# Kernel tuning notes

Measured on AMD Instinct MI355X. Metric: run time of the kernel, lower is better.

Reference implementation:

```python
import jax, jax.numpy as jnp
import numpy as np
import math

B, S, D = 2, 2048, 1024
H, HKV, HD = 16, 4, 64
SF = 4
SD = HD // SF  # sparsity proj dim = 16
TEMP = 1.0
INIT_STD = 0.02


def rope(qk):
    # qk: [b, h, s, d]
    d = qk.shape[-1]
    theta = 1.0 / (10000.0 ** (jnp.arange(0, d, 2, dtype=jnp.float32) / d))  # [d/2]
    s = jnp.arange(qk.shape[2], dtype=jnp.float32)
    freqs = jnp.outer(s, theta)                     # [s, d/2]
    freqs = jnp.concatenate([freqs, freqs], -1)     # [s, d]
    qk1, qk2 = jnp.split(qk, 2, axis=-1)
    rot = jnp.concatenate([-qk2, qk1], -1)
    return qk * jnp.cos(freqs) + rot * jnp.sin(freqs)


def setup_inputs() -> dict:
    key = jax.random.key(0)
    ks = jax.random.split(key, 8)
    x = jax.random.normal(ks[0], (B, S, D), dtype=jnp.float32)
    Wq = jax.random.normal(ks[1], (D, D), dtype=jnp.float32) * INIT_STD
    Wk = jax.random.normal(ks[2], (HKV * HD, D), dtype=jnp.float32) * INIT_STD
    Wv = jax.random.normal(ks[3], (HKV * HD, D), dtype=jnp.float32) * INIT_STD
    Wo = jax.random.normal(ks[4], (D, D), dtype=jnp.float32) * INIT_STD
    bo = jnp.zeros((D,), dtype=jnp.float32)
    Ws = jax.random.normal(ks[5], (SD, HD), dtype=jnp.float32) * INIT_STD
    bs = jnp.zeros((SD,), dtype=jnp.float32)
    return {"x": x, "Wq": Wq, "Wk": Wk, "Wv": Wv, "Wo": Wo, "bo": bo, "Ws": Ws, "bs": bs}


def reference(x, Wq, Wk, Wv, Wo, bo, Ws, bs):
    b, s, _ = x.shape
    # projections (torch Linear: x @ W.T)
    q = (x @ Wq.T).reshape(b, s, H, HD).transpose(0, 2, 1, 3)     # [b,H,s,hd]
    k = (x @ Wk.T).reshape(b, s, HKV, HD).transpose(0, 2, 1, 3)   # [b,Hkv,s,hd]
    v = (x @ Wv.T).reshape(b, s, HKV, HD).transpose(0, 2, 1, 3)
    q = rope(q)
    k = rope(k)
    n_rep = H // HKV
    k = jnp.repeat(k, n_rep, axis=1)  # [b,H,s,hd]
    v = jnp.repeat(v, n_rep, axis=1)
    # low-rank sparsity gate
    q_sp = q @ Ws.T + bs              # [b,H,s,sd]
    k_sp = k @ Ws.T + bs
    sp_scores = jnp.einsum('bhid,bhjd->bhij', q_sp, k_sp) / math.sqrt(SD)
    gate = jax.nn.sigmoid(sp_scores / TEMP)
    attn = jnp.einsum('bhid,bhjd->bhij', q, k) / math.sqrt(HD)
    attn = attn * gate
    causal = jnp.triu(jnp.ones((s, s), dtype=bool), k=1)
    attn = jnp.where(causal, -jnp.inf, attn)
    w = jax.nn.softmax(attn, axis=-1)
    out = jnp.einsum('bhij,bhjd->bhid', w, v)               # [b,H,s,hd]
    out = out.transpose(0, 2, 1, 3).reshape(b, s, H * HD)   # [b,s,D]
    return out @ Wo.T + bo
```

## Files before the change

kernel.cpp:

```cpp
#include <hip/hip_runtime.h>
#include <math.h>

#define B_ 2
#define S_ 2048
#define D_ 1024
#define H_ 16
#define HKV_ 4
#define HD_ 64
#define SD_ 16

typedef __attribute__((ext_vector_type(8))) short bf16x8;
typedef __attribute__((ext_vector_type(4))) float f32x4;
typedef __attribute__((ext_vector_type(8))) unsigned short us8;
typedef __attribute__((ext_vector_type(4))) unsigned short us4;

#define LOG2E 1.4426950408889634f

__device__ __forceinline__ unsigned short f2bf(float f) {
  unsigned int u = __builtin_bit_cast(unsigned int, f);
  u += 0x7fffu + ((u >> 16) & 1u);
  return (unsigned short)(u >> 16);
}

__device__ __forceinline__ void gload16(const unsigned short* g, unsigned short* l) {
  __builtin_amdgcn_global_load_lds(
      (const __attribute__((address_space(1))) unsigned int*)g,
      (__attribute__((address_space(3))) unsigned int*)l, 16, 0, 0);
}

__global__ __launch_bounds__(256) void convert_bf16(
    const float* __restrict__ x, const float* __restrict__ wq,
    const float* __restrict__ wk, const float* __restrict__ wv,
    const float* __restrict__ wo, unsigned short* __restrict__ xb,
    unsigned short* __restrict__ wqkv, unsigned short* __restrict__ wob,
    int* __restrict__ ctr) {
  const int blk = blockIdx.x;
  if (blk == 0 && threadIdx.x == 0) *ctr = 0;
  const float* src;
  unsigned short* dst;
  int off;
  if (blk < 2048)      { src = x;  dst = xb;             off = blk * 2048; }
  else if (blk < 2560) { src = wq; dst = wqkv;           off = (blk - 2048) * 2048; }
  else if (blk < 2688) { src = wk; dst = wqkv + 1048576; off = (blk - 2560) * 2048; }
  else if (blk < 2816) { src = wv; dst = wqkv + 1310720; off = (blk - 2688) * 2048; }
  else                 { src = wo; dst = wob;            off = (blk - 2816) * 2048; }
  const int i = off + threadIdx.x * 8;
  float4 a = *(const float4*)(src + i);
  float4 b = *(const float4*)(src + i + 4);
  us8 o;
  o[0] = f2bf(a.x); o[1] = f2bf(a.y); o[2] = f2bf(a.z); o[3] = f2bf(a.w);
  o[4] = f2bf(b.x); o[5] = f2bf(b.y); o[6] = f2bf(b.z); o[7] = f2bf(b.w);
  *(us8*)(dst + i) = o;
}

__global__ __launch_bounds__(256) void gemm_bf16(
    const unsigned short* __restrict__ A, const unsigned short* __restrict__ Bm,
    const float* __restrict__ bias, float* __restrict__ C, int N) {
  __shared__ unsigned short As[64 * 64];
  __shared__ unsigned short Bs[128 * 64];
  const int tid = threadIdx.x;
  const int w = tid >> 6, lane = tid & 63;
  const int nm = lane & 15, quad = lane >> 4;
  const int m0 = blockIdx.y * 64, n0 = blockIdx.x * 128;
  const int wn = w * 32;

  f32x4 acc[4][2] = {};
  int arow[2], acol[2], brow[4], bcol[4];
#pragma unroll
  for (int it = 0; it < 2; ++it) {
    int s = it * 256 + tid;
    arow[it] = s >> 3;
    acol[it] = ((s & 7) ^ (arow[it] & 7)) * 8;
  }
#pragma unroll
  for (int it = 0; it < 4; ++it) {
    int s = it * 256 + tid;
    brow[it] = s >> 3;
    bcol[it] = ((s & 7) ^ (brow[it] & 7)) * 8;
  }

  for (int k0 = 0; k0 < 1024; k0 += 64) {
    __syncthreads();
#pragma unroll
    for (int it = 0; it < 2; ++it)
      gload16(A + (size_t)(m0 + arow[it]) * 1024 + k0 + acol[it],
              &As[(it * 256 + w * 64) * 8]);
#pragma unroll
    for (int it = 0; it < 4; ++it)
      gload16(Bm + (size_t)(n0 + brow[it]) * 1024 + k0 + bcol[it],
              &Bs[(it * 256 + w * 64) * 8]);
    __syncthreads();

#pragma unroll
    for (int ks = 0; ks < 2; ++ks) {
      const int cq = ks * 4 + quad;
      bf16x8 af[4], bfr[2];
#pragma unroll
      for (int mi = 0; mi < 4; ++mi) {
        const int m = mi * 16 + nm;
        af[mi] = *(const bf16x8*)&As[(m * 8 + (cq ^ (m & 7))) * 8];
      }
#pragma unroll
      for (int ni = 0; ni < 2; ++ni) {
        const int n = wn + ni * 16 + nm;
        bfr[ni] = *(const bf16x8*)&Bs[(n * 8 + (cq ^ (n & 7))) * 8];
      }
#pragma unroll
      for (int mi = 0; mi < 4; ++mi)
#pragma unroll
        for (int ni = 0; ni < 2; ++ni)
          acc[mi][ni] = __builtin_amdgcn_mfma_f32_16x16x32_bf16(
              af[mi], bfr[ni], acc[mi][ni], 0, 0, 0);
    }
  }

  float bv[2] = {0.f, 0.f};
  if (bias) {
#pragma unroll
    for (int ni = 0; ni < 2; ++ni) bv[ni] = bias[n0 + wn + ni * 16 + nm];
  }
#pragma unroll
  for (int mi = 0; mi < 4; ++mi) {
#pragma unroll
    for (int r = 0; r < 4; ++r) {
      const int row = m0 + mi * 16 + quad * 4 + r;
      float* crow = C + (size_t)row * N + n0 + wn + nm;
#pragma unroll
      for (int ni = 0; ni < 2; ++ni) crow[ni * 16] = acc[mi][ni][r] + bv[ni];
    }
  }
}

__global__ __launch_bounds__(256) void rope_scatter(
    const float* __restrict__ P, const float* __restrict__ Ws,
    const float* __restrict__ bs, unsigned short* __restrict__ qh,
    unsigned short* __restrict__ kh, unsigned short* __restrict__ qsp,
    unsigned short* __restrict__ ksp) {
  __shared__ float wsl[16 * 64];
  __shared__ float bsl[16];
  __shared__ float rbuf[4][64];
  const int tid = threadIdx.x;
  const int row = blockIdx.x;
  const int b = row >> 11;
  const int s = row & 2047;
  {
    *(float4*)&wsl[tid * 4] = *(const float4*)&Ws[tid * 4];
    if (tid < 16) bsl[tid] = bs[tid];
  }
  __syncthreads();
  const int w = tid >> 6, lane = tid & 63;
  const int i = lane & 31, halfu = lane >> 5;
  const float theta = powf(10000.f, -((float)(2 * i) * (1.f / 64.f)));
  const float f = (float)s * theta;
  const float cf = cosf(f);
  const float sf = sinf(f);
  for (int slot = w; slot < 20; slot += 4) {
    float val = P[(size_t)row * 1536 + slot * 64 + lane];
    float partner = __shfl_xor(val, 32);
    float rot = halfu ? partner : -partner;
    float r = val * cf + rot * sf;
    unsigned short* dst;
    unsigned short* spdst;
    float qscale, spscale;
    if (slot < 16) {
      dst = qh + ((size_t)(b * 16 + slot) * 2048 + s) * 64;
      spdst = qsp + ((size_t)(b * 16 + slot) * 2048 + s) * 16;
      qscale = 0.125f * LOG2E; spscale = 0.25f * LOG2E;
    } else {
      int hh = slot - 16;
      dst = kh + ((size_t)(b * 4 + hh) * 2048 + s) * 64;
      spdst = ksp + ((size_t)(b * 4 + hh) * 2048 + s) * 16;
      qscale = 1.f; spscale = 1.f;
    }
    dst[lane] = f2bf(r * qscale);
    rbuf[w][lane] = r;
    int p = lane >> 4, j = lane & 15;
    float partial = 0.f;
#pragma unroll
    for (int t = 0; t < 16; ++t)
      partial += wsl[j * 64 + p * 16 + t] * rbuf[w][p * 16 + t];
    partial += __shfl_xor(partial, 16);
    partial += __shfl_xor(partial, 32);
    if (p == 0) spdst[j] = f2bf((partial + bsl[j]) * spscale);
  }
}

__global__ __launch_bounds__(256) void v_transpose(
    const float* __restrict__ proj, unsigned short* __restrict__ vt) {
  __shared__ unsigned short t_[64 * 72];
  const int bkv = blockIdx.y;
  const int s0 = blockIdx.x * 64;
  const int b = bkv >> 2, hkv = bkv & 3;
  const int tid = threadIdx.x;
  const int sl = tid >> 2;
  const int c0 = (tid & 3) * 16;
  const float* src = proj + ((size_t)b * 2048 + s0 + sl) * 1536 + 1280 + hkv * 64 + c0;
  us8 o0, o1;
#pragma unroll
  for (int t = 0; t < 8; ++t) { o0[t] = f2bf(src[t]); o1[t] = f2bf(src[8 + t]); }
  *(us8*)&t_[sl * 72 + c0] = o0;
  *(us8*)&t_[sl * 72 + c0 + 8] = o1;
  __syncthreads();
  const int d = tid >> 2;
  const int sc_ = (tid & 3) * 16;
  us8 w0, w1;
#pragma unroll
  for (int t = 0; t < 8; ++t) w0[t] = t_[(sc_ + t) * 72 + d];
#pragma unroll
  for (int t = 0; t < 8; ++t) w1[t] = t_[(sc_ + 8 + t) * 72 + d];
  unsigned short* dst = vt + (size_t)bkv * 131072 + (size_t)d * 2048 + s0 + sc_;
  *(us8*)dst = w0;
  *(us8*)(dst + 8) = w1;
}

__global__ __launch_bounds__(256) void attn_kernel(
    const unsigned short* __restrict__ qh, const unsigned short* __restrict__ kh,
    const unsigned short* __restrict__ vt, const unsigned short* __restrict__ qsp,
    const unsigned short* __restrict__ ksp, int* __restrict__ ctr,
    unsigned short* __restrict__ ao) {
  __shared__ unsigned short Ks[64 * 64];
  __shared__ unsigned short Vs[64 * 64];
  __shared__ unsigned short Ksp[64 * 16];
  __shared__ unsigned short Pw[4][16 * 64];
  __shared__ int item_s;

  const int tid = threadIdx.x;
  const int w = tid >> 6;
  const int lane = tid & 63;
  const int nm = lane & 15;
  const int quad = lane >> 4;

  int srow_[2], scol_[2];
#pragma unroll
  for (int rd = 0; rd < 2; ++rd) {
    int Lc = rd * 256 + w * 64 + lane;
    int r = Lc >> 3;
    srow_[rd] = r;
    scol_[rd] = ((Lc & 7) ^ (r & 7)) * 8;
  }
  unsigned short* pw = &Pw[w][0];

  for (;;) {
    if (tid == 0) item_s = atomicAdd(ctr, 1);
    __syncthreads();
    const int t = item_s;
    if (t >= 1024) break;
    const int qx = 31 - (t >> 5);
    const int bh = t & 31;
    const int b = bh >> 4, h = bh & 15;
    const int hkv = h >> 2;
    const size_t kbase = (size_t)(b * 4 + hkv) * 2048 * 64;
    const size_t vbase = (size_t)(b * 4 + hkv) * 131072;
    const size_t kspb = (size_t)(b * 4 + hkv) * 2048 * 16;
    const int q0 = qx * 64;
    const int qrow0 = q0 + w * 16;

    const size_t qb = ((size_t)(b * 16 + h) * 2048 + qrow0 + nm) * 64;
    bf16x8 qa0 = *(const bf16x8*)(qh + qb + quad * 8);
    bf16x8 qa1 = *(const bf16x8*)(qh + qb + 32 + quad * 8);
    bf16x8 qspa = {0, 0, 0, 0, 0, 0, 0, 0};
    if (quad < 2)
      qspa = *(const bf16x8*)(qsp + ((size_t)(b * 16 + h) * 2048 + qrow0 + nm) * 16 + quad * 8);

    float l_r[4] = {0.f, 0.f, 0.f, 0.f};
    f32x4 O[4] = {{0.f, 0.f, 0.f, 0.f}, {0.f, 0.f, 0.f, 0.f},
                  {0.f, 0.f, 0.f, 0.f}, {0.f, 0.f, 0.f, 0.f}};

    const int ntile = qx + 1;
    for (int jt = 0; jt < ntile; ++jt) {
      const int j0 = jt * 64;
      __syncthreads();
#pragma unroll
      for (int rd = 0; rd < 2; ++rd) {
        gload16(kh + kbase + (size_t)(j0 + srow_[rd]) * 64 + scol_[rd],
                &Ks[(rd * 256 + w * 64) * 8]);
        gload16(vt + vbase + (size_t)srow_[rd] * 2048 + j0 + scol_[rd],
                &Vs[(rd * 256 + w * 64) * 8]);
      }
      if (w < 2) {
        const int Lc = w * 64 + lane;
        gload16(ksp + kspb + (size_t)(j0 + (Lc >> 1)) * 16 + (Lc & 1) * 8,
                &Ksp[w * 512]);
      }
      __syncthreads();

      const bool needmask = (j0 + 63 > qrow0);
#pragma unroll
      for (int st = 0; st < 4; ++st) {
        const int krow = st * 16 + nm;
        const int r7 = krow & 7;
        bf16x8 kb0 = *(const bf16x8*)&Ks[(krow * 8 + (quad ^ r7)) * 8];
        bf16x8 kb1 = *(const bf16x8*)&Ks[(krow * 8 + ((4 + quad) ^ r7)) * 8];
        bf16x8 gb = *(const bf16x8*)&Ksp[(krow * 2 + (quad & 1)) * 8];
        f32x4 z = {0.f, 0.f, 0.f, 0.f};
        f32x4 s = __builtin_amdgcn_mfma_f32_16x16x32_bf16(qa0, kb0, z, 0, 0, 0);
        s = __builtin_amdgcn_mfma_f32_16x16x32_bf16(qa1, kb1, s, 0, 0, 0);
        f32x4 g = __builtin_amdgcn_mfma_f32_16x16x32_bf16(qspa, gb, z, 0, 0, 0);
#pragma unroll
        for (int r = 0; r < 4; ++r) {
          float gate = 1.f / (1.f + exp2f(-g[r]));
          float v = s[r] * gate;
          if (needmask) {
            const int col = j0 + st * 16 + nm;
            const int rowg = qrow0 + quad * 4 + r;
            v = (col > rowg) ? -INFINITY : v;
          }
          float p = exp2f(v);
          l_r[r] += p;
          const int prow = quad * 4 + r;
          const int chunk = (st * 2 + (nm >> 3)) ^ (prow & 7);
          pw[(prow * 8 + chunk) * 8 + (nm & 7)] = f2bf(p);
        }
      }

#pragma unroll
      for (int c = 0; c < 2; ++c) {
        const int gc = c * 4 + quad;
        bf16x8 pa = *(const bf16x8*)&pw[(nm * 8 + (gc ^ (nm & 7))) * 8];
#pragma unroll
        for (int dt = 0; dt < 4; ++dt) {
          const int vrow = dt * 16 + nm;
          bf16x8 vb = *(const bf16x8*)&Vs[(vrow * 8 + (gc ^ (vrow & 7))) * 8];
          O[dt] = __builtin_amdgcn_mfma_f32_16x16x32_bf16(pa, vb, O[dt], 0, 0, 0);
        }
      }
    }

#pragma unroll
    for (int r = 0; r < 4; ++r) {
      float v = l_r[r];
      v += __shfl_xor(v, 1);
      v += __shfl_xor(v, 2);
      v += __shfl_xor(v, 4);
      v += __shfl_xor(v, 8);
      const float inv = 1.f / v;
      const int rowg = qrow0 + quad * 4 + r;
      unsigned short* orow = ao + ((size_t)b * 2048 + rowg) * 1024 + h * 64 + nm;
#pragma unroll
      for (int dt = 0; dt < 4; ++dt) orow[dt * 16] = f2bf(O[dt][r] * inv);
    }
  }
}

extern "C" void kernel_launch(void* const* d_in, const int* in_sizes, int n_in,
                              void* d_out, int out_size, void* d_ws,
                              size_t ws_size, hipStream_t stream) {
  const float* x = (const float*)d_in[0];
  const float* Wq = (const float*)d_in[1];
  const float* Wk = (const float*)d_in[2];
  const float* Wv = (const float*)d_in[3];
  const float* Wo = (const float*)d_in[4];
  const float* bo = (const float*)d_in[5];
  const float* Ws = (const float*)d_in[6];
  const float* bs = (const float*)d_in[7];
  float* out = (float*)d_out;

  char* wsb = (char*)d_ws;
  float* proj = (float*)wsb;
  unsigned short* aob = (unsigned short*)wsb;
  unsigned short* qh   = (unsigned short*)(wsb + 25165824);
  unsigned short* kh   = (unsigned short*)(wsb + 33554432);
  unsigned short* vtb  = (unsigned short*)(wsb + 35651584);
  unsigned short* qsp  = (unsigned short*)(wsb + 37748736);
  unsigned short* ksp  = (unsigned short*)(wsb + 39845888);
  unsigned short* xb   = (unsigned short*)(wsb + 40370176);
  unsigned short* wqkv = (unsigned short*)(wsb + 48758784);
  unsigned short* wob  = (unsigned short*)(wsb + 51904512);
  int* ctr             = (int*)(wsb + 54001664);

  convert_bf16<<<dim3(3328), 256, 0, stream>>>(x, Wq, Wk, Wv, Wo, xb, wqkv, wob, ctr);
  gemm_bf16<<<dim3(12, 64), 256, 0, stream>>>(xb, wqkv, nullptr, proj, 1536);
  rope_scatter<<<dim3(4096), 256, 0, stream>>>(proj, Ws, bs, qh, kh, qsp, ksp);
  v_transpose<<<dim3(32, 8), 256, 0, stream>>>(proj, vtb);
  attn_kernel<<<dim3(1024), 256, 0, stream>>>(qh, kh, vtb, qsp, ksp, ctr, aob);
  gemm_bf16<<<dim3(8, 64), 256, 0, stream>>>(aob, wob, bo, out, 1024);
}
```

Before: 228.3 us.

## Split attention KV range into two halves and combine partials in a separate kernel

Each query-tile work item is split into two items that cover the first and second halves of the causal KV tiles. This doubles parallelism and shortens the longest items, which improves load balance in the persistent atomic-counter scheduler. Each half writes unnormalized bf16 partial outputs and row sums to workspace. A new combine kernel adds the two halves and normalizes them. The cost is extra partial-output traffic, one more launch, duplicated Q loads, and rounding unnormalized partials to bf16.

```diff
diff --git a/kernel.cpp b/kernel.cpp
--- a/kernel.cpp
+++ b/kernel.cpp
@@ -20,6 +20,9 @@
   unsigned int u = __builtin_bit_cast(unsigned int, f);
   u += 0x7fffu + ((u >> 16) & 1u);
   return (unsigned short)(u >> 16);
+}
+__device__ __forceinline__ float bf2f(unsigned short x) {
+  return __builtin_bit_cast(float, (unsigned int)x << 16);
 }
 
 __device__ __forceinline__ void gload16(const unsigned short* g, unsigned short* l) {
@@ -217,7 +220,7 @@
     const unsigned short* __restrict__ qh, const unsigned short* __restrict__ kh,
     const unsigned short* __restrict__ vt, const unsigned short* __restrict__ qsp,
     const unsigned short* __restrict__ ksp, int* __restrict__ ctr,
-    unsigned short* __restrict__ ao) {
+    unsigned short* __restrict__ opart, float* __restrict__ lpart) {
   __shared__ unsigned short Ks[64 * 64];
   __shared__ unsigned short Vs[64 * 64];
   __shared__ unsigned short Ksp[64 * 16];
@@ -244,9 +247,11 @@
     if (tid == 0) item_s = atomicAdd(ctr, 1);
     __syncthreads();
     const int t = item_s;
-    if (t >= 1024) break;
-    const int qx = 31 - (t >> 5);
+    if (t >= 2048) break;
+    const int u = t >> 5;
     const int bh = t & 31;
+    const int qx = 31 - (u >> 1);
+    const int half = u & 1;
     const int b = bh >> 4, h = bh & 15;
     const int hkv = h >> 2;
     const size_t kbase = (size_t)(b * 4 + hkv) * 2048 * 64;
@@ -254,6 +259,10 @@
     const size_t kspb = (size_t)(b * 4 + hkv) * 2048 * 16;
     const int q0 = qx * 64;
     const int qrow0 = q0 + w * 16;
+    const int nt = qx + 1;
+    const int hsplit = (nt + 1) >> 1;
+    const int jt0 = half ? hsplit : 0;
+    const int jt1 = half ? nt : hsplit;
 
     const size_t qb = ((size_t)(b * 16 + h) * 2048 + qrow0 + nm) * 64;
     bf16x8 qa0 = *(const bf16x8*)(qh + qb + quad * 8);
@@ -266,8 +275,7 @@
     f32x4 O[4] = {{0.f, 0.f, 0.f, 0.f}, {0.f, 0.f, 0.f, 0.f},
                   {0.f, 0.f, 0.f, 0.f}, {0.f, 0.f, 0.f, 0.f}};
 
-    const int ntile = qx + 1;
-    for (int jt = 0; jt < ntile; ++jt) {
+    for (int jt = jt0; jt < jt1; ++jt) {
       const int j0 = jt * 64;
       __syncthreads();
 #pragma unroll
@@ -333,13 +341,40 @@
       v += __shfl_xor(v, 2);
       v += __shfl_xor(v, 4);
       v += __shfl_xor(v, 8);
-      const float inv = 1.f / v;
-      const int rowg = qrow0 + quad * 4 + r;
-      unsigned short* orow = ao + ((size_t)b * 2048 + rowg) * 1024 + h * 64 + nm;
-#pragma unroll
-      for (int dt = 0; dt < 4; ++dt) orow[dt * 16] = f2bf(O[dt][r] * inv);
+      const int prow = w * 16 + quad * 4 + r;
+      unsigned short* orow = opart + ((size_t)t * 64 + prow) * 64 + nm;
+#pragma unroll
+      for (int dt = 0; dt < 4; ++dt) orow[dt * 16] = f2bf(O[dt][r]);
+      if (nm == 0) lpart[t * 64 + prow] = v;
     }
   }
+}
+
+__global__ __launch_bounds__(256) void attn_combine(
+    const unsigned short* __restrict__ opart, const float* __restrict__ lpart,
+    unsigned short* __restrict__ ao) {
+  const int bh = blockIdx.x, qx = blockIdx.y;
+  const int b = bh >> 4, h = bh & 15;
+  const int t = threadIdx.x;
+  const int row = t >> 2, d0 = (t & 3) * 16;
+  const size_t p0 = (size_t)((31 - qx) * 2) * 32 + bh;
+  const size_t p1 = p0 + 32;
+  const unsigned short* a0 = opart + (p0 * 64 + row) * 64 + d0;
+  const unsigned short* a1 = opart + (p1 * 64 + row) * 64 + d0;
+  const float inv = 1.f / (lpart[p0 * 64 + row] + lpart[p1 * 64 + row]);
+  us8 x0 = *(const us8*)a0;
+  us8 x1 = *(const us8*)(a0 + 8);
+  us8 y0 = *(const us8*)a1;
+  us8 y1 = *(const us8*)(a1 + 8);
+  us8 o0, o1;
+#pragma unroll
+  for (int i = 0; i < 8; ++i) {
+    o0[i] = f2bf((bf2f(x0[i]) + bf2f(y0[i])) * inv);
+    o1[i] = f2bf((bf2f(x1[i]) + bf2f(y1[i])) * inv);
+  }
+  unsigned short* dst = ao + ((size_t)b * 2048 + qx * 64 + row) * 1024 + h * 64 + d0;
+  *(us8*)dst = o0;
+  *(us8*)(dst + 8) = o1;
 }
 
 extern "C" void kernel_launch(void* const* d_in, const int* in_sizes, int n_in,
@@ -357,13 +392,15 @@
 
   char* wsb = (char*)d_ws;
   float* proj = (float*)wsb;
-  unsigned short* aob = (unsigned short*)wsb;
+  unsigned short* aob  = (unsigned short*)wsb;
+  unsigned short* opart = (unsigned short*)(wsb + 8388608);
   unsigned short* qh   = (unsigned short*)(wsb + 25165824);
   unsigned short* kh   = (unsigned short*)(wsb + 33554432);
   unsigned short* vtb  = (unsigned short*)(wsb + 35651584);
   unsigned short* qsp  = (unsigned short*)(wsb + 37748736);
   unsigned short* ksp  = (unsigned short*)(wsb + 39845888);
   unsigned short* xb   = (unsigned short*)(wsb + 40370176);
+  float* lpart         = (float*)(wsb + 40370176);
   unsigned short* wqkv = (unsigned short*)(wsb + 48758784);
   unsigned short* wob  = (unsigned short*)(wsb + 51904512);
   int* ctr             = (int*)(wsb + 54001664);
@@ -372,6 +409,7 @@
   gemm_bf16<<<dim3(12, 64), 256, 0, stream>>>(xb, wqkv, nullptr, proj, 1536);
   rope_scatter<<<dim3(4096), 256, 0, stream>>>(proj, Ws, bs, qh, kh, qsp, ksp);
   v_transpose<<<dim3(32, 8), 256, 0, stream>>>(proj, vtb);
-  attn_kernel<<<dim3(1024), 256, 0, stream>>>(qh, kh, vtb, qsp, ksp, ctr, aob);
+  attn_kernel<<<dim3(1536), 256, 0, stream>>>(qh, kh, vtb, qsp, ksp, ctr, opart, lpart);
+  attn_combine<<<dim3(32, 32), 256, 0, stream>>>(opart, lpart, aob);
   gemm_bf16<<<dim3(8, 64), 256, 0, stream>>>(aob, wob, bo, out, 1024);
 }
```

Result: slower. 238.7 us (+4.6%).

## Split attention KV tile across two wave groups with 512-thread blocks

Applied to the files above, without the earlier changes.

The attention kernel now runs 512 threads per block. Eight waves split each 64-key tile into two 32-key halves per 16-row query group, and the partial O and row sums are combined through shared memory at the end. Fully masked 16-key sub-tiles are skipped and zero-filled in the P buffer. The aim is more waves in flight and less causal work on diagonal tiles, at the cost of an extra cross-wave reduction and more synchronisation per work item.

```diff
diff --git a/kernel.cpp b/kernel.cpp
--- a/kernel.cpp
+++ b/kernel.cpp
@@ -213,15 +213,14 @@
   *(us8*)(dst + 8) = w1;
 }
 
-__global__ __launch_bounds__(256) void attn_kernel(
+__global__ __launch_bounds__(512) void attn_kernel(
     const unsigned short* __restrict__ qh, const unsigned short* __restrict__ kh,
     const unsigned short* __restrict__ vt, const unsigned short* __restrict__ qsp,
     const unsigned short* __restrict__ ksp, int* __restrict__ ctr,
     unsigned short* __restrict__ ao) {
-  __shared__ unsigned short Ks[64 * 64];
-  __shared__ unsigned short Vs[64 * 64];
+  __shared__ unsigned short KV[2][64 * 64];
   __shared__ unsigned short Ksp[64 * 16];
-  __shared__ unsigned short Pw[4][16 * 64];
+  __shared__ unsigned short Pw[8][16 * 32];
   __shared__ int item_s;
 
   const int tid = threadIdx.x;
@@ -229,15 +228,11 @@
   const int lane = tid & 63;
   const int nm = lane & 15;
   const int quad = lane >> 4;
-
-  int srow_[2], scol_[2];
-#pragma unroll
-  for (int rd = 0; rd < 2; ++rd) {
-    int Lc = rd * 256 + w * 64 + lane;
-    int r = Lc >> 3;
-    srow_[rd] = r;
-    scol_[rd] = ((Lc & 7) ^ (r & 7)) * 8;
-  }
+  const int kh2 = w >> 2;
+  const int qg = w & 3;
+
+  const int r_ = tid >> 3;
+  const int gc_ = ((tid & 7) ^ (r_ & 7));
   unsigned short* pw = &Pw[w][0];
 
   for (;;) {
@@ -252,8 +247,7 @@
     const size_t kbase = (size_t)(b * 4 + hkv) * 2048 * 64;
     const size_t vbase = (size_t)(b * 4 + hkv) * 131072;
     const size_t kspb = (size_t)(b * 4 + hkv) * 2048 * 16;
-    const int q0 = qx * 64;
-    const int qrow0 = q0 + w * 16;
+    const int qrow0 = qx * 64 + qg * 16;
 
     const size_t qb = ((size_t)(b * 16 + h) * 2048 + qrow0 + nm) * 64;
     bf16x8 qa0 = *(const bf16x8*)(qh + qb + quad * 8);
@@ -270,74 +264,94 @@
     for (int jt = 0; jt < ntile; ++jt) {
       const int j0 = jt * 64;
       __syncthreads();
-#pragma unroll
-      for (int rd = 0; rd < 2; ++rd) {
-        gload16(kh + kbase + (size_t)(j0 + srow_[rd]) * 64 + scol_[rd],
-                &Ks[(rd * 256 + w * 64) * 8]);
-        gload16(vt + vbase + (size_t)srow_[rd] * 2048 + j0 + scol_[rd],
-                &Vs[(rd * 256 + w * 64) * 8]);
-      }
-      if (w < 2) {
-        const int Lc = w * 64 + lane;
-        gload16(ksp + kspb + (size_t)(j0 + (Lc >> 1)) * 16 + (Lc & 1) * 8,
+      gload16(kh + kbase + (size_t)(j0 + r_) * 64 + gc_ * 8, &KV[0][w * 512]);
+      gload16(vt + vbase + (size_t)r_ * 2048 + j0 + gc_ * 8, &KV[1][w * 512]);
+      if (w < 2)
+        gload16(ksp + kspb + (size_t)(j0 + (tid >> 1)) * 16 + (tid & 1) * 8,
                 &Ksp[w * 512]);
-      }
       __syncthreads();
 
-      const bool needmask = (j0 + 63 > qrow0);
-#pragma unroll
-      for (int st = 0; st < 4; ++st) {
-        const int krow = st * 16 + nm;
+#pragma unroll
+      for (int st2 = 0; st2 < 2; ++st2) {
+        const int kcol0 = kh2 * 32 + st2 * 16;
+        if (j0 + kcol0 > qrow0 + 15) {
+#pragma unroll
+          for (int r = 0; r < 4; ++r) {
+            const int prow = quad * 4 + r;
+            const int chunk = (st2 * 2 + (nm >> 3)) ^ (prow & 3);
+            pw[(prow * 4 + chunk) * 8 + (nm & 7)] = 0;
+          }
+          continue;
+        }
+        const int krow = kcol0 + nm;
         const int r7 = krow & 7;
-        bf16x8 kb0 = *(const bf16x8*)&Ks[(krow * 8 + (quad ^ r7)) * 8];
-        bf16x8 kb1 = *(const bf16x8*)&Ks[(krow * 8 + ((4 + quad) ^ r7)) * 8];
+        bf16x8 kb0 = *(const bf16x8*)&KV[0][(krow * 8 + (quad ^ r7)) * 8];
+        bf16x8 kb1 = *(const bf16x8*)&KV[0][(krow * 8 + ((4 + quad) ^ r7)) * 8];
         bf16x8 gb = *(const bf16x8*)&Ksp[(krow * 2 + (quad & 1)) * 8];
         f32x4 z = {0.f, 0.f, 0.f, 0.f};
         f32x4 s = __builtin_amdgcn_mfma_f32_16x16x32_bf16(qa0, kb0, z, 0, 0, 0);
         s = __builtin_amdgcn_mfma_f32_16x16x32_bf16(qa1, kb1, s, 0, 0, 0);
         f32x4 g = __builtin_amdgcn_mfma_f32_16x16x32_bf16(qspa, gb, z, 0, 0, 0);
+        const bool needmask = (j0 + kcol0 + 15 > qrow0);
 #pragma unroll
         for (int r = 0; r < 4; ++r) {
           float gate = 1.f / (1.f + exp2f(-g[r]));
           float v = s[r] * gate;
           if (needmask) {
-            const int col = j0 + st * 16 + nm;
+            const int col = j0 + kcol0 + nm;
             const int rowg = qrow0 + quad * 4 + r;
             v = (col > rowg) ? -INFINITY : v;
           }
           float p = exp2f(v);
           l_r[r] += p;
           const int prow = quad * 4 + r;
-          const int chunk = (st * 2 + (nm >> 3)) ^ (prow & 7);
-          pw[(prow * 8 + chunk) * 8 + (nm & 7)] = f2bf(p);
+          const int chunk = (st2 * 2 + (nm >> 3)) ^ (prow & 3);
+          pw[(prow * 4 + chunk) * 8 + (nm & 7)] = f2bf(p);
         }
       }
 
-#pragma unroll
-      for (int c = 0; c < 2; ++c) {
-        const int gc = c * 4 + quad;
-        bf16x8 pa = *(const bf16x8*)&pw[(nm * 8 + (gc ^ (nm & 7))) * 8];
+      {
+        bf16x8 pa = *(const bf16x8*)&pw[(nm * 4 + (quad ^ (nm & 3))) * 8];
 #pragma unroll
         for (int dt = 0; dt < 4; ++dt) {
           const int vrow = dt * 16 + nm;
-          bf16x8 vb = *(const bf16x8*)&Vs[(vrow * 8 + (gc ^ (vrow & 7))) * 8];
+          const int gvc = kh2 * 4 + quad;
+          bf16x8 vb = *(const bf16x8*)&KV[1][(vrow * 8 + (gvc ^ (vrow & 7))) * 8];
           O[dt] = __builtin_amdgcn_mfma_f32_16x16x32_bf16(pa, vb, O[dt], 0, 0, 0);
         }
       }
     }
 
-#pragma unroll
-    for (int r = 0; r < 4; ++r) {
-      float v = l_r[r];
-      v += __shfl_xor(v, 1);
-      v += __shfl_xor(v, 2);
-      v += __shfl_xor(v, 4);
-      v += __shfl_xor(v, 8);
-      const float inv = 1.f / v;
-      const int rowg = qrow0 + quad * 4 + r;
-      unsigned short* orow = ao + ((size_t)b * 2048 + rowg) * 1024 + h * 64 + nm;
-#pragma unroll
-      for (int dt = 0; dt < 4; ++dt) orow[dt * 16] = f2bf(O[dt][r] * inv);
+    __syncthreads();
+    float* osc = (float*)&KV[0][0];
+    float* lsc = (float*)&Pw[0][0];
+    if (kh2 == 1) {
+#pragma unroll
+      for (int r = 0; r < 4; ++r) {
+        const int prow = qg * 16 + quad * 4 + r;
+#pragma unroll
+        for (int dt = 0; dt < 4; ++dt)
+          osc[prow * 64 + dt * 16 + nm] = O[dt][r];
+        lsc[prow * 16 + nm] = l_r[r];
+      }
+    }
+    __syncthreads();
+    if (kh2 == 0) {
+#pragma unroll
+      for (int r = 0; r < 4; ++r) {
+        const int prow = qg * 16 + quad * 4 + r;
+        float lv = l_r[r] + lsc[prow * 16 + nm];
+        lv += __shfl_xor(lv, 1);
+        lv += __shfl_xor(lv, 2);
+        lv += __shfl_xor(lv, 4);
+        lv += __shfl_xor(lv, 8);
+        const float inv = 1.f / lv;
+        const int rowg = qx * 64 + prow;
+        unsigned short* orow = ao + ((size_t)b * 2048 + rowg) * 1024 + h * 64 + nm;
+#pragma unroll
+        for (int dt = 0; dt < 4; ++dt)
+          orow[dt * 16] = f2bf((O[dt][r] + osc[prow * 64 + dt * 16 + nm]) * inv);
+      }
     }
   }
 }
@@ -357,7 +371,7 @@
 
   char* wsb = (char*)d_ws;
   float* proj = (float*)wsb;
-  unsigned short* aob = (unsigned short*)wsb;
+  unsigned short* aob  = (unsigned short*)wsb;
   unsigned short* qh   = (unsigned short*)(wsb + 25165824);
   unsigned short* kh   = (unsigned short*)(wsb + 33554432);
   unsigned short* vtb  = (unsigned short*)(wsb + 35651584);
@@ -372,6 +386,6 @@
   gemm_bf16<<<dim3(12, 64), 256, 0, stream>>>(xb, wqkv, nullptr, proj, 1536);
   rope_scatter<<<dim3(4096), 256, 0, stream>>>(proj, Ws, bs, qh, kh, qsp, ksp);
   v_transpose<<<dim3(32, 8), 256, 0, stream>>>(proj, vtb);
-  attn_kernel<<<dim3(1024), 256, 0, stream>>>(qh, kh, vtb, qsp, ksp, ctr, aob);
+  attn_kernel<<<dim3(512), 512, 0, stream>>>(qh, kh, vtb, qsp, ksp, ctr, aob);
   gemm_bf16<<<dim3(8, 64), 256, 0, stream>>>(aob, wob, bo, out, 1024);
 }
```

New measurement: 222.3 us. -2.6%, faster.
